# Kernel optimization log

Measured on AMD Instinct MI355X. Metric: run time of the kernel, lower is better.

## Reference

```python
import jax, jax.numpy as jnp
import numpy as np

# Tree / model dimensions
L = 1024          # number of leaves (batch rows of x)
F = 128           # num_features
H = 128           # num_dense_units
C = 10            # output_dim (num classes)
N = 2 * L - 1     # full binary tree node count
SPLICE = [0, F*H, F*H+H, F*H+H+H*H, F*H+2*H+H*H, F*H+2*H+H*H+H*C, F*H+2*H+H*H+H*C+C]
D = SPLICE[-1]    # 34314 = flattened sub-MLP weight count (layer_shape)
MIN_DIST = 1e-7


def setup_inputs() -> dict:
    key = jax.random.key(0)
    k1, k2, k3 = jax.random.split(key, 3)
    x = jax.random.normal(k1, (L, F), dtype=jnp.float32)
    # per-node AdditionLayer weight vectors (trainable deltas)
    W = jax.random.normal(k2, (N, D), dtype=jnp.float32) * 0.02
    heights = jax.random.uniform(k3, (N,), dtype=jnp.float32)
    p = (np.arange(N) - 1) // 2
    p[0] = 0  # root self-parent; root is excluded from the mut-distance term
    parent = jnp.asarray(p, dtype=jnp.int32)
    leaf_idx = jnp.arange(L - 1, N, dtype=jnp.int32)  # leaves in traversal order
    return {"x": x, "W": W, "heights": heights, "parent": parent, "leaf_idx": leaf_idx}


def reference(x, W, heights, parent, leaf_idx):
    n = W.shape[0]
    depth = int(np.log2(n + 1))
    # Effective weights per node = sum of AdditionLayer deltas along root->node path.
    # Level-by-level parent gather (parents at level d-1 are already accumulated).
    eff = W
    for d in range(1, depth):
        s, e = 2 ** d - 1, 2 ** (d + 1) - 1
        eff = eff.at[s:e].add(eff[parent[s:e]])

    # delta_tensor: root uses squared diff vs zero input (= sum(W_root^2));
    # every other node: curr - input = W_node, so sum|W_node| / mut_distance.
    mut = jnp.maximum(jnp.abs(heights - heights[parent]), MIN_DIST)  # [n]
    l1 = jnp.sum(jnp.abs(W), axis=1)                                 # [n]
    delta = jnp.sum(W[0] ** 2) + jnp.sum(l1[1:] / mut[1:])
    delta = jnp.reshape(delta, (1,))

    # Leaf sub-MLP: splice each leaf's effective weight vector into kernels/biases
    wl = eff[leaf_idx]                                  # [L, D]
    Lf = wl.shape[0]
    W0 = wl[:, SPLICE[0]:SPLICE[1]].reshape(Lf, F, H)
    b0 = wl[:, SPLICE[1]:SPLICE[2]]
    W1 = wl[:, SPLICE[2]:SPLICE[3]].reshape(Lf, H, H)
    b1 = wl[:, SPLICE[3]:SPLICE[4]]
    W2 = wl[:, SPLICE[4]:SPLICE[5]].reshape(Lf, H, C)
    b2 = wl[:, SPLICE[5]:SPLICE[6]]
    h = jax.nn.relu(jnp.einsum('lf,lfh->lh', x, W0) + b0)
    h = jax.nn.relu(jnp.einsum('lh,lhk->lk', h, W1) + b1)
    out = jax.nn.softmax(jnp.einsum('lh,lhc->lc', h, W2) + b2, axis=-1)
    return (out, delta)
```

## Files before the change

### kernel.cpp

```cpp
#include <hip/hip_runtime.h>

#define LN 1024
#define FF 128
#define HH 128
#define CC 10
#define DD 34314
#define OFF_W0 0
#define OFF_B0 16384
#define OFF_W1 16512
#define OFF_B1 32896
#define OFF_W2 33024
#define OFF_B2 34304

__global__ void init_delta(float* delta) { *delta = 0.f; }

__device__ __forceinline__ float invmut(const float* h, int node, int par) {
    return 1.f / fmaxf(fabsf(h[node] - h[par]), 1e-7f);
}

__global__ __launch_bounds__(1024, 4)
__attribute__((amdgpu_waves_per_eu(4, 4)))
void fused_kernel(const float* __restrict__ W,
                  const float* __restrict__ x,
                  const float* __restrict__ heights,
                  float* __restrict__ out,
                  float* __restrict__ delta_out) {
    const int bid  = blockIdx.x;
    const int m    = ((bid & 7) << 5) | (bid >> 3);
    const int tid  = threadIdx.x;
    const int lane = tid & 63;
    const int wv   = tid >> 6;
    const int j2   = lane;

    int path[9];
    {
        int n = 255 + m;
#pragma unroll
        for (int k = 0; k < 9; ++k) { path[k] = n; n = (n - 1) >> 1; }
    }
    const float* R[15];
#pragma unroll
    for (int k = 0; k < 9; ++k) R[k] = W + (size_t)path[k] * DD;
    const int n9a = 511 + 2 * m, n9b = n9a + 1;
    R[9]  = W + (size_t)n9a * DD;
    R[10] = W + (size_t)n9b * DD;
#pragma unroll
    for (int q = 0; q < 4; ++q) R[11 + q] = W + (size_t)(1023 + 4 * m + q) * DD;

    float wgt[15];
#pragma unroll
    for (int k = 0; k < 8; ++k)
        wgt[k] = ((m & ((1 << k) - 1)) == 0) ? invmut(heights, path[k], path[k + 1]) : 0.f;
    wgt[8]  = 0.f;
    wgt[9]  = invmut(heights, n9a, path[0]);
    wgt[10] = invmut(heights, n9b, path[0]);
#pragma unroll
    for (int q = 0; q < 4; ++q)
        wgt[11 + q] = invmut(heights, 1023 + 4 * m + q, (q < 2) ? n9a : n9b);
    const float sqmask = (m == 0) ? 1.f : 0.f;

    __shared__ float ins[4][HH];
    __shared__ float part[4][16][HH];
    __shared__ float lgts[4][CC];
    __shared__ float red[16];

    if (tid < 512) { const int q = tid >> 7, t = tid & 127; ins[q][t] = x[(4 * m + q) * FF + t]; }
    if (tid < 4 * CC) ((float*)lgts)[tid] = 0.f;

    float dacc = 0.f, sacc = 0.f;
    __syncthreads();

#pragma unroll
    for (int layer = 0; layer < 2; ++layer) {
        const int offW = layer ? OFF_W1 : OFF_W0;
        const int offB = layer ? OFF_B1 : OFF_B0;
        const float2* S2[15];
#pragma unroll
        for (int r = 0; r < 15; ++r) S2[r] = reinterpret_cast<const float2*>(R[r] + offW);

        float yx[4], yy[4];
#pragma unroll
        for (int q = 0; q < 4; ++q) { yx[q] = 0.f; yy[q] = 0.f; }

#pragma unroll 2
        for (int i = 0; i < 8; ++i) {
            const int f   = (wv << 3) + i;
            const int off = (f << 6) + j2;
            float ex = 0.f, ey = 0.f;
#pragma unroll
            for (int k = 0; k < 9; ++k) {
                const float2 w = S2[k][off];
                ex += w.x; ey += w.y;
                dacc += (fabsf(w.x) + fabsf(w.y)) * wgt[k];
                if (k == 8) sacc += w.x * w.x + w.y * w.y;
            }
            const float2 wa0 = S2[9][off];
            const float2 wa1 = S2[10][off];
            dacc += (fabsf(wa0.x) + fabsf(wa0.y)) * wgt[9];
            dacc += (fabsf(wa1.x) + fabsf(wa1.y)) * wgt[10];
#pragma unroll
            for (int q = 0; q < 4; ++q) {
                const float2 wb = S2[11 + q][off];
                dacc += (fabsf(wb.x) + fabsf(wb.y)) * wgt[11 + q];
                const float2 wa = (q < 2) ? wa0 : wa1;
                const float xv = ins[q][f];
                yx[q] += xv * (ex + wa.x + wb.x);
                yy[q] += xv * (ey + wa.y + wb.y);
            }
        }
#pragma unroll
        for (int q = 0; q < 4; ++q)
            *reinterpret_cast<float2*>(&part[q][wv][2 * j2]) = make_float2(yx[q], yy[q]);
        __syncthreads();

        if (tid < 512) {
            const int q = tid >> 7, col = tid & 127;
            float eb = 0.f;
#pragma unroll
            for (int k = 0; k < 9; ++k) {
                const float v = R[k][offB + col];
                eb += v;
                if (q == 0) { dacc += fabsf(v) * wgt[k]; if (k == 8) sacc += v * v; }
            }
            const float a0 = R[9][offB + col];
            const float a1 = R[10][offB + col];
            if (q == 0) dacc += fabsf(a0) * wgt[9];
            if (q == 2) dacc += fabsf(a1) * wgt[10];
            const float bq = R[11 + q][offB + col];
            dacc += fabsf(bq) * wgt[11 + q];
            float s = eb + ((q < 2) ? a0 : a1) + bq;
#pragma unroll
            for (int w = 0; w < 16; ++w) s += part[q][w][col];
            ins[q][col] = fmaxf(s, 0.f);
        }
        __syncthreads();
    }

    {
        const float2* S2[15];
#pragma unroll
        for (int r = 0; r < 15; ++r) S2[r] = reinterpret_cast<const float2*>(R[r] + OFF_W2);
        if (tid < 640) {
            const int h  = tid / 5;
            const int c0 = (tid - 5 * h) * 2;
            float ex = 0.f, ey = 0.f;
#pragma unroll
            for (int k = 0; k < 9; ++k) {
                const float2 w = S2[k][tid];
                ex += w.x; ey += w.y;
                dacc += (fabsf(w.x) + fabsf(w.y)) * wgt[k];
                if (k == 8) sacc += w.x * w.x + w.y * w.y;
            }
            const float2 wa0 = S2[9][tid];
            const float2 wa1 = S2[10][tid];
            dacc += (fabsf(wa0.x) + fabsf(wa0.y)) * wgt[9];
            dacc += (fabsf(wa1.x) + fabsf(wa1.y)) * wgt[10];
#pragma unroll
            for (int q = 0; q < 4; ++q) {
                const float2 wb = S2[11 + q][tid];
                dacc += (fabsf(wb.x) + fabsf(wb.y)) * wgt[11 + q];
                const float2 wa = (q < 2) ? wa0 : wa1;
                const float hv = ins[q][h];
                atomicAdd(&lgts[q][c0],     hv * (ex + wa.x + wb.x));
                atomicAdd(&lgts[q][c0 + 1], hv * (ey + wa.y + wb.y));
            }
        }
        __syncthreads();
        if (tid < CC) {
            float eb = 0.f;
#pragma unroll
            for (int k = 0; k < 9; ++k) {
                const float v = R[k][OFF_B2 + tid];
                eb += v;
                dacc += fabsf(v) * wgt[k];
                if (k == 8) sacc += v * v;
            }
            const float a0 = R[9][OFF_B2 + tid];
            const float a1 = R[10][OFF_B2 + tid];
            dacc += fabsf(a0) * wgt[9] + fabsf(a1) * wgt[10];
#pragma unroll
            for (int q = 0; q < 4; ++q) {
                const float bq = R[11 + q][OFF_B2 + tid];
                dacc += fabsf(bq) * wgt[11 + q];
                lgts[q][tid] += eb + ((q < 2) ? a0 : a1) + bq;
            }
        }
        __syncthreads();
    }

    if (tid < 4) {
        const int q = tid;
        float mx = lgts[q][0];
#pragma unroll
        for (int c = 1; c < CC; ++c) mx = fmaxf(mx, lgts[q][c]);
        float e[CC], s = 0.f;
#pragma unroll
        for (int c = 0; c < CC; ++c) { e[c] = expf(lgts[q][c] - mx); s += e[c]; }
        const float inv = 1.f / s;
#pragma unroll
        for (int c = 0; c < CC; ++c) out[(4 * m + q) * CC + c] = e[c] * inv;
    }

    float v = dacc + sacc * sqmask;
    for (int o = 32; o > 0; o >>= 1) v += __shfl_down(v, o);
    if (lane == 0) red[wv] = v;
    __syncthreads();
    if (tid == 0) {
        float s = 0.f;
#pragma unroll
        for (int w = 0; w < 16; ++w) s += red[w];
        atomicAdd(delta_out, s);
    }
}

extern "C" void kernel_launch(void* const* d_in, const int* in_sizes, int n_in,
                              void* d_out, int out_size, void* d_ws, size_t ws_size,
                              hipStream_t stream) {
    const float* x       = (const float*)d_in[0];
    const float* W       = (const float*)d_in[1];
    const float* heights = (const float*)d_in[2];

    float* out   = (float*)d_out;
    float* delta = (float*)d_out + LN * CC;

    init_delta<<<1, 1, 0, stream>>>(delta);
    fused_kernel<<<256, 1024, 0, stream>>>(W, x, heights, out, delta);
}
```

Baseline: 96.34 us.

## Stream layer weights through double-buffered LDS tiles via global_load_lds

Replaces direct per-thread float2 global loads of the 15 path/leaf weight rows with asynchronous global-to-LDS copies into a double-buffered shared tile. Each 1024-float tile of the next feature slice is prefetched while the current one is consumed, and the layer loop is no longer unrolled. The aim is to overlap memory latency with compute and cut register pressure. In exchange it adds about 120KB of shared memory per block and a barrier per tile, which limits occupancy to one block per CU and may add sync overhead.

After: 152.0 us. 57.8% more time.

```diff
diff --git a/kernel.cpp b/kernel.cpp
--- a/kernel.cpp
+++ b/kernel.cpp
@@ -11,6 +11,8 @@
 #define OFF_B1 32896
 #define OFF_W2 33024
 #define OFF_B2 34304
+#define TILE 1024
+#define NT 16
 
 __global__ void init_delta(float* delta) { *delta = 0.f; }
 
@@ -18,7 +20,7 @@
     return 1.f / fmaxf(fabsf(h[node] - h[par]), 1e-7f);
 }
 
-__global__ __launch_bounds__(1024, 4)
+__global__ __launch_bounds__(1024, 1)
 __attribute__((amdgpu_waves_per_eu(4, 4)))
 void fused_kernel(const float* __restrict__ W,
                   const float* __restrict__ x,
@@ -30,7 +32,6 @@
     const int tid  = threadIdx.x;
     const int lane = tid & 63;
     const int wv   = tid >> 6;
-    const int j2   = lane;
 
     int path[9];
     {
@@ -59,8 +60,8 @@
         wgt[11 + q] = invmut(heights, 1023 + 4 * m + q, (q < 2) ? n9a : n9b);
     const float sqmask = (m == 0) ? 1.f : 0.f;
 
+    __shared__ float buf[2][15][TILE];
     __shared__ float ins[4][HH];
-    __shared__ float part[4][16][HH];
     __shared__ float lgts[4][CC];
     __shared__ float red[16];
 
@@ -68,70 +69,82 @@
     if (tid < 4 * CC) ((float*)lgts)[tid] = 0.f;
 
     float dacc = 0.f, sacc = 0.f;
-    __syncthreads();
-
-#pragma unroll
+
+    const int fg  = tid >> 7;
+    const int col = tid & 127;
+
+#pragma unroll 1
     for (int layer = 0; layer < 2; ++layer) {
         const int offW = layer ? OFF_W1 : OFF_W0;
         const int offB = layer ? OFF_B1 : OFF_B0;
-        const float2* S2[15];
-#pragma unroll
-        for (int r = 0; r < 15; ++r) S2[r] = reinterpret_cast<const float2*>(R[r] + offW);
-
-        float yx[4], yy[4];
-#pragma unroll
-        for (int q = 0; q < 4; ++q) { yx[q] = 0.f; yy[q] = 0.f; }
-
-#pragma unroll 2
-        for (int i = 0; i < 8; ++i) {
-            const int f   = (wv << 3) + i;
-            const int off = (f << 6) + j2;
-            float ex = 0.f, ey = 0.f;
+
+        float yacc[4] = {0.f, 0.f, 0.f, 0.f};
+
+#pragma unroll
+        for (int j = 0; j < 15; ++j) {
+            const int id = wv * 15 + j, r = id >> 4, c = id & 15;
+            const float* gsrc = R[r] + offW + 0 * TILE + c * 64 + lane;
+            __builtin_amdgcn_global_load_lds(
+                (const __attribute__((address_space(1))) void*)gsrc,
+                (__attribute__((address_space(3))) void*)&buf[0][r][c * 64], 4, 0, 0);
+        }
+
+#pragma unroll 1
+        for (int t = 0; t < NT; ++t) {
+            const int cur = t & 1;
+            __syncthreads();
+            if (t + 1 < NT) {
+#pragma unroll
+                for (int j = 0; j < 15; ++j) {
+                    const int id = wv * 15 + j, r = id >> 4, c = id & 15;
+                    const float* gsrc = R[r] + offW + (t + 1) * TILE + c * 64 + lane;
+                    __builtin_amdgcn_global_load_lds(
+                        (const __attribute__((address_space(1))) void*)gsrc,
+                        (__attribute__((address_space(3))) void*)&buf[cur ^ 1][r][c * 64], 4, 0, 0);
+                }
+            }
+            const int f = t * 8 + fg;
+            float w[15];
+#pragma unroll
+            for (int r = 0; r < 15; ++r) w[r] = buf[cur][r][tid];
+            float e = 0.f;
+#pragma unroll
+            for (int k = 0; k < 9; ++k) { e += w[k]; dacc += fabsf(w[k]) * wgt[k]; }
+            sacc += w[8] * w[8];
+            dacc += fabsf(w[9]) * wgt[9] + fabsf(w[10]) * wgt[10];
+            const float xv0 = ins[0][f], xv1 = ins[1][f], xv2 = ins[2][f], xv3 = ins[3][f];
+            dacc += fabsf(w[11]) * wgt[11] + fabsf(w[12]) * wgt[12]
+                  + fabsf(w[13]) * wgt[13] + fabsf(w[14]) * wgt[14];
+            yacc[0] += xv0 * (e + w[9]  + w[11]);
+            yacc[1] += xv1 * (e + w[9]  + w[12]);
+            yacc[2] += xv2 * (e + w[10] + w[13]);
+            yacc[3] += xv3 * (e + w[10] + w[14]);
+        }
+        __syncthreads();
+
+        float* scratch = &buf[0][0][0];
+#pragma unroll
+        for (int q = 0; q < 4; ++q) scratch[q * 1024 + tid] = yacc[q];
+        __syncthreads();
+        if (tid < 512) {
+            const int q = tid >> 7, c2 = tid & 127;
+            float eb = 0.f;
 #pragma unroll
             for (int k = 0; k < 9; ++k) {
-                const float2 w = S2[k][off];
-                ex += w.x; ey += w.y;
-                dacc += (fabsf(w.x) + fabsf(w.y)) * wgt[k];
-                if (k == 8) sacc += w.x * w.x + w.y * w.y;
-            }
-            const float2 wa0 = S2[9][off];
-            const float2 wa1 = S2[10][off];
-            dacc += (fabsf(wa0.x) + fabsf(wa0.y)) * wgt[9];
-            dacc += (fabsf(wa1.x) + fabsf(wa1.y)) * wgt[10];
-#pragma unroll
-            for (int q = 0; q < 4; ++q) {
-                const float2 wb = S2[11 + q][off];
-                dacc += (fabsf(wb.x) + fabsf(wb.y)) * wgt[11 + q];
-                const float2 wa = (q < 2) ? wa0 : wa1;
-                const float xv = ins[q][f];
-                yx[q] += xv * (ex + wa.x + wb.x);
-                yy[q] += xv * (ey + wa.y + wb.y);
-            }
-        }
-#pragma unroll
-        for (int q = 0; q < 4; ++q)
-            *reinterpret_cast<float2*>(&part[q][wv][2 * j2]) = make_float2(yx[q], yy[q]);
-        __syncthreads();
-
-        if (tid < 512) {
-            const int q = tid >> 7, col = tid & 127;
-            float eb = 0.f;
-#pragma unroll
-            for (int k = 0; k < 9; ++k) {
-                const float v = R[k][offB + col];
+                const float v = R[k][offB + c2];
                 eb += v;
                 if (q == 0) { dacc += fabsf(v) * wgt[k]; if (k == 8) sacc += v * v; }
             }
-            const float a0 = R[9][offB + col];
-            const float a1 = R[10][offB + col];
+            const float a0 = R[9][offB + c2];
+            const float a1 = R[10][offB + c2];
             if (q == 0) dacc += fabsf(a0) * wgt[9];
             if (q == 2) dacc += fabsf(a1) * wgt[10];
-            const float bq = R[11 + q][offB + col];
+            const float bq = R[11 + q][offB + c2];
             dacc += fabsf(bq) * wgt[11 + q];
             float s = eb + ((q < 2) ? a0 : a1) + bq;
 #pragma unroll
-            for (int w = 0; w < 16; ++w) s += part[q][w][col];
-            ins[q][col] = fmaxf(s, 0.f);
+            for (int g = 0; g < 8; ++g) s += scratch[q * 1024 + g * 128 + c2];
+            ins[q][c2] = fmaxf(s, 0.f);
         }
         __syncthreads();
     }
```

## Precompute level-5 ancestor sums in a separate kernel to cut per-block reads

Applied to the files above, without the earlier changes.

Adds a pre-pass kernel that sums the W rows along each path from the root down to the 32 level-5 nodes and writes them to workspace. The same pass accumulates those ancestors' delta contributions. The main kernel then reads 1 precomputed row plus 3 path rows instead of 9 ancestor rows per block, which cuts redundant global and L2 traffic. The cost is an extra launch and a workspace write and read of 32 rows.

Result: faster. 83.37 us, median of 2 (-13.5%).

```diff
diff --git a/kernel.cpp b/kernel.cpp
--- a/kernel.cpp
+++ b/kernel.cpp
@@ -5,6 +5,8 @@
 #define HH 128
 #define CC 10
 #define DD 34314
+#define DD2 17157
+#define CHK 2145
 #define OFF_W0 0
 #define OFF_B0 16384
 #define OFF_W1 16512
@@ -18,9 +20,65 @@
     return 1.f / fmaxf(fabsf(h[node] - h[par]), 1e-7f);
 }
 
+__global__ __launch_bounds__(1024) void eff5_kernel(const float* __restrict__ W,
+                                                    const float* __restrict__ heights,
+                                                    float* __restrict__ eff,
+                                                    float* __restrict__ delta_out) {
+    const int bid = blockIdx.x;
+    const int n5  = bid >> 3;
+    const int ck  = bid & 7;
+    const int tid = threadIdx.x, lane = tid & 63, wv = tid >> 6;
+
+    int p[6];
+    p[0] = 31 + n5;
+#pragma unroll
+    for (int k = 1; k < 6; ++k) p[k] = (p[k - 1] - 1) >> 1;
+
+    const float2* S[6];
+#pragma unroll
+    for (int k = 0; k < 6; ++k) S[k] = reinterpret_cast<const float2*>(W + (size_t)p[k] * DD);
+    float2* E = reinterpret_cast<float2*>(eff + (size_t)n5 * DD);
+
+    float wgt[6];
+#pragma unroll
+    for (int k = 0; k < 5; ++k)
+        wgt[k] = ((n5 & ((1 << k) - 1)) == 0) ? invmut(heights, p[k], p[k + 1]) : 0.f;
+    wgt[5] = 0.f;
+    const float sqm = (n5 == 0) ? 1.f : 0.f;
+
+    float dacc = 0.f, sacc = 0.f;
+    const int lo = ck * CHK;
+    const int hi = min(lo + CHK, DD2);
+#pragma unroll 1
+    for (int i = lo + tid; i < hi; i += 1024) {
+        float ex = 0.f, ey = 0.f;
+#pragma unroll
+        for (int k = 0; k < 6; ++k) {
+            const float2 w = S[k][i];
+            ex += w.x; ey += w.y;
+            dacc += (fabsf(w.x) + fabsf(w.y)) * wgt[k];
+            if (k == 5) sacc += w.x * w.x + w.y * w.y;
+        }
+        E[i] = make_float2(ex, ey);
+    }
+
+    __shared__ float red[16];
+    float v = dacc + sacc * sqm;
+    for (int o = 32; o > 0; o >>= 1) v += __shfl_down(v, o);
+    if (lane == 0) red[wv] = v;
+    __syncthreads();
+    if (tid == 0) {
+        float s = 0.f;
+#pragma unroll
+        for (int w = 0; w < 16; ++w) s += red[w];
+        atomicAdd(delta_out, s);
+    }
+}
+
 __global__ __launch_bounds__(1024, 4)
 __attribute__((amdgpu_waves_per_eu(4, 4)))
 void fused_kernel(const float* __restrict__ W,
+                  const float* __restrict__ eff,
                   const float* __restrict__ x,
                   const float* __restrict__ heights,
                   float* __restrict__ out,
@@ -32,32 +90,35 @@
     const int wv   = tid >> 6;
     const int j2   = lane;
 
-    int path[9];
-    {
-        int n = 255 + m;
-#pragma unroll
-        for (int k = 0; k < 9; ++k) { path[k] = n; n = (n - 1) >> 1; }
-    }
-    const float* R[15];
-#pragma unroll
-    for (int k = 0; k < 9; ++k) R[k] = W + (size_t)path[k] * DD;
+    const int l8 = 255 + m;
+    const int l7 = (l8 - 1) >> 1;
+    const int l6 = (l7 - 1) >> 1;
+    const int l5 = (l6 - 1) >> 1;
+
+    const float* RE = eff + (size_t)(m >> 3) * DD;
+    const float* RP[3];
+    RP[0] = W + (size_t)l8 * DD;
+    RP[1] = W + (size_t)l7 * DD;
+    RP[2] = W + (size_t)l6 * DD;
     const int n9a = 511 + 2 * m, n9b = n9a + 1;
-    R[9]  = W + (size_t)n9a * DD;
-    R[10] = W + (size_t)n9b * DD;
-#pragma unroll
-    for (int q = 0; q < 4; ++q) R[11 + q] = W + (size_t)(1023 + 4 * m + q) * DD;
-
-    float wgt[15];
-#pragma unroll
-    for (int k = 0; k < 8; ++k)
-        wgt[k] = ((m & ((1 << k) - 1)) == 0) ? invmut(heights, path[k], path[k + 1]) : 0.f;
-    wgt[8]  = 0.f;
-    wgt[9]  = invmut(heights, n9a, path[0]);
-    wgt[10] = invmut(heights, n9b, path[0]);
+    const float* RA[2];
+    RA[0] = W + (size_t)n9a * DD;
+    RA[1] = W + (size_t)n9b * DD;
+    const float* RB[4];
+#pragma unroll
+    for (int q = 0; q < 4; ++q) RB[q] = W + (size_t)(1023 + 4 * m + q) * DD;
+
+    float wgtP[3];
+    wgtP[0] = invmut(heights, l8, l7);
+    wgtP[1] = ((m & 1) == 0) ? invmut(heights, l7, l6) : 0.f;
+    wgtP[2] = ((m & 3) == 0) ? invmut(heights, l6, l5) : 0.f;
+    float wgtA[2];
+    wgtA[0] = invmut(heights, n9a, l8);
+    wgtA[1] = invmut(heights, n9b, l8);
+    float wgtB[4];
 #pragma unroll
     for (int q = 0; q < 4; ++q)
-        wgt[11 + q] = invmut(heights, 1023 + 4 * m + q, (q < 2) ? n9a : n9b);
-    const float sqmask = (m == 0) ? 1.f : 0.f;
+        wgtB[q] = invmut(heights, 1023 + 4 * m + q, (q < 2) ? n9a : n9b);
 
     __shared__ float ins[4][HH];
     __shared__ float part[4][16][HH];
@@ -67,16 +128,23 @@
     if (tid < 512) { const int q = tid >> 7, t = tid & 127; ins[q][t] = x[(4 * m + q) * FF + t]; }
     if (tid < 4 * CC) ((float*)lgts)[tid] = 0.f;
 
-    float dacc = 0.f, sacc = 0.f;
+    float dacc = 0.f;
     __syncthreads();
 
 #pragma unroll
     for (int layer = 0; layer < 2; ++layer) {
         const int offW = layer ? OFF_W1 : OFF_W0;
         const int offB = layer ? OFF_B1 : OFF_B0;
-        const float2* S2[15];
-#pragma unroll
-        for (int r = 0; r < 15; ++r) S2[r] = reinterpret_cast<const float2*>(R[r] + offW);
+        const float2* SE = reinterpret_cast<const float2*>(RE + offW);
+        const float2* SP[3];
+#pragma unroll
+        for (int r = 0; r < 3; ++r) SP[r] = reinterpret_cast<const float2*>(RP[r] + offW);
+        const float2* SA[2];
+#pragma unroll
+        for (int r = 0; r < 2; ++r) SA[r] = reinterpret_cast<const float2*>(RA[r] + offW);
+        const float2* SB[4];
+#pragma unroll
+        for (int r = 0; r < 4; ++r) SB[r] = reinterpret_cast<const float2*>(RB[r] + offW);
 
         float yx[4], yy[4];
 #pragma unroll
@@ -86,22 +154,22 @@
         for (int i = 0; i < 8; ++i) {
             const int f   = (wv << 3) + i;
             const int off = (f << 6) + j2;
-            float ex = 0.f, ey = 0.f;
-#pragma unroll
-            for (int k = 0; k < 9; ++k) {
-                const float2 w = S2[k][off];
+            const float2 we = SE[off];
+            float ex = we.x, ey = we.y;
+#pragma unroll
+            for (int k = 0; k < 3; ++k) {
+                const float2 w = SP[k][off];
                 ex += w.x; ey += w.y;
-                dacc += (fabsf(w.x) + fabsf(w.y)) * wgt[k];
-                if (k == 8) sacc += w.x * w.x + w.y * w.y;
-            }
-            const float2 wa0 = S2[9][off];
-            const float2 wa1 = S2[10][off];
-            dacc += (fabsf(wa0.x) + fabsf(wa0.y)) * wgt[9];
-            dacc += (fabsf(wa1.x) + fabsf(wa1.y)) * wgt[10];
+                dacc += (fabsf(w.x) + fabsf(w.y)) * wgtP[k];
+            }
+            const float2 wa0 = SA[0][off];
+            const float2 wa1 = SA[1][off];
+            dacc += (fabsf(wa0.x) + fabsf(wa0.y)) * wgtA[0];
+            dacc += (fabsf(wa1.x) + fabsf(wa1.y)) * wgtA[1];
 #pragma unroll
             for (int q = 0; q < 4; ++q) {
-                const float2 wb = S2[11 + q][off];
-                dacc += (fabsf(wb.x) + fabsf(wb.y)) * wgt[11 + q];
+                const float2 wb = SB[q][off];
+                dacc += (fabsf(wb.x) + fabsf(wb.y)) * wgtB[q];
                 const float2 wa = (q < 2) ? wa0 : wa1;
                 const float xv = ins[q][f];
                 yx[q] += xv * (ex + wa.x + wb.x);
@@ -115,19 +183,18 @@
 
         if (tid < 512) {
             const int q = tid >> 7, col = tid & 127;
-            float eb = 0.f;
-#pragma unroll
-            for (int k = 0; k < 9; ++k) {
-                const float v = R[k][offB + col];
-                eb += v;
-                if (q == 0) { dacc += fabsf(v) * wgt[k]; if (k == 8) sacc += v * v; }
-            }
-            const float a0 = R[9][offB + col];
-            const float a1 = R[10][offB + col];
-            if (q == 0) dacc += fabsf(a0) * wgt[9];
-            if (q == 2) dacc += fabsf(a1) * wgt[10];
-            const float bq = R[11 + q][offB + col];
-            dacc += fabsf(bq) * wgt[11 + q];
+            const float p0 = RP[0][offB + col];
+            const float p1 = RP[1][offB + col];
+            const float p2 = RP[2][offB + col];
+            float eb = RE[offB + col] + p0 + p1 + p2;
+            if (q == 0)
+                dacc += fabsf(p0) * wgtP[0] + fabsf(p1) * wgtP[1] + fabsf(p2) * wgtP[2];
+            const float a0 = RA[0][offB + col];
+            const float a1 = RA[1][offB + col];
+            if (q == 0) dacc += fabsf(a0) * wgtA[0];
+            if (q == 2) dacc += fabsf(a1) * wgtA[1];
+            const float bq = RB[q][offB + col];
+            dacc += fabsf(bq) * wgtB[q];
             float s = eb + ((q < 2) ? a0 : a1) + bq;
 #pragma unroll
             for (int w = 0; w < 16; ++w) s += part[q][w][col];
@@ -137,28 +204,35 @@
     }
 
     {
-        const float2* S2[15];
-#pragma unroll
-        for (int r = 0; r < 15; ++r) S2[r] = reinterpret_cast<const float2*>(R[r] + OFF_W2);
+        const float2* SE = reinterpret_cast<const float2*>(RE + OFF_W2);
+        const float2* SP[3];
+#pragma unroll
+        for (int r = 0; r < 3; ++r) SP[r] = reinterpret_cast<const float2*>(RP[r] + OFF_W2);
+        const float2* SA[2];
+#pragma unroll
+        for (int r = 0; r < 2; ++r) SA[r] = reinterpret_cast<const float2*>(RA[r] + OFF_W2);
+        const float2* SB[4];
+#pragma unroll
+        for (int r = 0; r < 4; ++r) SB[r] = reinterpret_cast<const float2*>(RB[r] + OFF_W2);
         if (tid < 640) {
             const int h  = tid / 5;
             const int c0 = (tid - 5 * h) * 2;
-            float ex = 0.f, ey = 0.f;
-#pragma unroll
-            for (int k = 0; k < 9; ++k) {
-                const float2 w = S2[k][tid];
+            const float2 we = SE[tid];
+            float ex = we.x, ey = we.y;
+#pragma unroll
+            for (int k = 0; k < 3; ++k) {
+                const float2 w = SP[k][tid];
                 ex += w.x; ey += w.y;
-                dacc += (fabsf(w.x) + fabsf(w.y)) * wgt[k];
-                if (k == 8) sacc += w.x * w.x + w.y * w.y;
-            }
-            const float2 wa0 = S2[9][tid];
-            const float2 wa1 = S2[10][tid];
-            dacc += (fabsf(wa0.x) + fabsf(wa0.y)) * wgt[9];
-            dacc += (fabsf(wa1.x) + fabsf(wa1.y)) * wgt[10];
+                dacc += (fabsf(w.x) + fabsf(w.y)) * wgtP[k];
+            }
+            const float2 wa0 = SA[0][tid];
+            const float2 wa1 = SA[1][tid];
+            dacc += (fabsf(wa0.x) + fabsf(wa0.y)) * wgtA[0];
+            dacc += (fabsf(wa1.x) + fabsf(wa1.y)) * wgtA[1];
 #pragma unroll
             for (int q = 0; q < 4; ++q) {
-                const float2 wb = S2[11 + q][tid];
-                dacc += (fabsf(wb.x) + fabsf(wb.y)) * wgt[11 + q];
+                const float2 wb = SB[q][tid];
+                dacc += (fabsf(wb.x) + fabsf(wb.y)) * wgtB[q];
                 const float2 wa = (q < 2) ? wa0 : wa1;
                 const float hv = ins[q][h];
                 atomicAdd(&lgts[q][c0],     hv * (ex + wa.x + wb.x));
@@ -167,21 +241,18 @@
         }
         __syncthreads();
         if (tid < CC) {
-            float eb = 0.f;
-#pragma unroll
-            for (int k = 0; k < 9; ++k) {
-                const float v = R[k][OFF_B2 + tid];
-                eb += v;
-                dacc += fabsf(v) * wgt[k];
-                if (k == 8) sacc += v * v;
-            }
-            const float a0 = R[9][OFF_B2 + tid];
-            const float a1 = R[10][OFF_B2 + tid];
-            dacc += fabsf(a0) * wgt[9] + fabsf(a1) * wgt[10];
+            const float p0 = RP[0][OFF_B2 + tid];
+            const float p1 = RP[1][OFF_B2 + tid];
+            const float p2 = RP[2][OFF_B2 + tid];
+            float eb = RE[OFF_B2 + tid] + p0 + p1 + p2;
+            dacc += fabsf(p0) * wgtP[0] + fabsf(p1) * wgtP[1] + fabsf(p2) * wgtP[2];
+            const float a0 = RA[0][OFF_B2 + tid];
+            const float a1 = RA[1][OFF_B2 + tid];
+            dacc += fabsf(a0) * wgtA[0] + fabsf(a1) * wgtA[1];
 #pragma unroll
             for (int q = 0; q < 4; ++q) {
-                const float bq = R[11 + q][OFF_B2 + tid];
-                dacc += fabsf(bq) * wgt[11 + q];
+                const float bq = RB[q][OFF_B2 + tid];
+                dacc += fabsf(bq) * wgtB[q];
                 lgts[q][tid] += eb + ((q < 2) ? a0 : a1) + bq;
             }
         }
@@ -201,7 +272,7 @@
         for (int c = 0; c < CC; ++c) out[(4 * m + q) * CC + c] = e[c] * inv;
     }
 
-    float v = dacc + sacc * sqmask;
+    float v = dacc;
     for (int o = 32; o > 0; o >>= 1) v += __shfl_down(v, o);
     if (lane == 0) red[wv] = v;
     __syncthreads();
@@ -222,7 +293,9 @@
 
     float* out   = (float*)d_out;
     float* delta = (float*)d_out + LN * CC;
+    float* eff   = (float*)d_ws;
 
     init_delta<<<1, 1, 0, stream>>>(delta);
-    fused_kernel<<<256, 1024, 0, stream>>>(W, x, heights, out, delta);
+    eff5_kernel<<<256, 1024, 0, stream>>>(W, heights, eff, delta);
+    fused_kernel<<<256, 1024, 0, stream>>>(W, eff, x, heights, out, delta);
 }
```
